# Kernel optimization log

Hardware: AMD Instinct MI355X
Metric: run time of the kernel (lower is better)

## Reference

```python
import jax, jax.numpy as jnp
import numpy as np

H = 64  # hidden_size


def _lstm_layer(xs, Wih, Whh, bih, bhh):
    # xs: (S, B, in_dim). PyTorch gate order: i, f, g, o.
    S, B, _ = xs.shape
    b = bih + bhh  # (4H,)
    # Precompute input projections for all timesteps (one big GEMM)
    x_proj = jnp.einsum('sbi,gi->sbg', xs, Wih) + b  # (S, B, 4H)

    def step(carry, xp_t):
        h, c = carry
        gates = xp_t + h @ Whh.T  # (B, 4H)
        i, f, g, o = jnp.split(gates, 4, axis=-1)
        i = jax.nn.sigmoid(i)
        f = jax.nn.sigmoid(f)
        g = jnp.tanh(g)
        o = jax.nn.sigmoid(o)
        c = f * c + i * g
        h = o * jnp.tanh(c)
        return (h, c), h

    h0 = jnp.zeros((B, H), dtype=xs.dtype)
    c0 = jnp.zeros((B, H), dtype=xs.dtype)
    _, ys = jax.lax.scan(step, (h0, c0), x_proj)
    return ys  # (S, B, H)


def setup_inputs() -> dict:
    key = jax.random.key(0)
    ks = jax.random.split(key, 16)
    scale = 1.0 / np.sqrt(H)  # PyTorch uniform(-1/sqrt(H), 1/sqrt(H)) scale

    def u(k, shape):
        return jax.random.uniform(k, shape, jnp.float32, -scale, scale)

    inp = {
        'x': jax.random.normal(ks[0], (512, 2048, 4), dtype=jnp.float32),
        # layer 0: input_size=4
        'Wih0': u(ks[1], (4 * H, 4)), 'Whh0': u(ks[2], (4 * H, H)),
        'bih0': u(ks[3], (4 * H,)), 'bhh0': u(ks[4], (4 * H,)),
        # layers 1,2: input_size=H
        'Wih1': u(ks[5], (4 * H, H)), 'Whh1': u(ks[6], (4 * H, H)),
        'bih1': u(ks[7], (4 * H,)), 'bhh1': u(ks[8], (4 * H,)),
        'Wih2': u(ks[9], (4 * H, H)), 'Whh2': u(ks[10], (4 * H, H)),
        'bih2': u(ks[11], (4 * H,)), 'bhh2': u(ks[12], (4 * H,)),
        # fc: Linear(64, 2)
        'fc_w': u(ks[13], (2, H)), 'fc_b': u(ks[14], (2,)),
    }
    return inp


def reference(x, Wih0, Whh0, bih0, bhh0, Wih1, Whh1, bih1, bhh1,
              Wih2, Whh2, bih2, bhh2, fc_w, fc_b):
    xs = jnp.transpose(x, (1, 0, 2))  # (S, B, 4) -- x.permute(1,0,2)
    h = _lstm_layer(xs, Wih0, Whh0, bih0, bhh0)
    h = _lstm_layer(h, Wih1, Whh1, bih1, bhh1)
    h = _lstm_layer(h, Wih2, Whh2, bih2, bhh2)
    last = h[-1]  # (B, H) -- out[-1]
    return last @ fc_w.T + fc_b  # (B, 2)
```

## Files before the change

### kernel.cpp

```cpp
#include <hip/hip_runtime.h>

#define SS 2048
#define BATCH 512
#define NB 2
#define NT 512

typedef float f2 __attribute__((ext_vector_type(2)));

__device__ __forceinline__ float fast_rcp(float a) { return __builtin_amdgcn_rcpf(a); }
__device__ __forceinline__ float fast_exp2(float a) { return __builtin_amdgcn_exp2f(a); }

__device__ __forceinline__ f2 pk_fma(f2 a, f2 b, f2 c) {
  return __builtin_elementwise_fma(a, b, c);
}
__device__ __forceinline__ f2 pk_mul(f2 a, f2 b) { return a * b; }

template <int CTRL>
__device__ __forceinline__ float dpp_add(float v) {
  const int sh = __builtin_amdgcn_update_dpp(0, __float_as_int(v), CTRL, 0xf, 0xf, true);
  return v + __int_as_float(sh);
}
template <int CTRL>
__device__ __forceinline__ float dpp_mov(float v) {
  return __int_as_float(__builtin_amdgcn_update_dpp(0, __float_as_int(v), CTRL, 0xf, 0xf, true));
}

__device__ __forceinline__ void lds_barrier() {
  asm volatile("s_waitcnt lgkmcnt(0)\n\ts_barrier" ::: "memory");
}

__device__ __forceinline__ void ld8(const float* p, f2 (&hv)[4]) {
  const float4 A = *(const float4*)p;
  const float4 B = *(const float4*)(p + 4);
  hv[0] = f2{A.x, A.y}; hv[1] = f2{A.z, A.w};
  hv[2] = f2{B.x, B.y}; hv[3] = f2{B.z, B.w};
}

__device__ __forceinline__ void mv8p_first(const f2 (&w)[4][4], const f2 (&hv)[4],
                                           f2 (&acc)[4]) {
#pragma unroll
  for (int g = 0; g < 4; ++g) {
    acc[g] = pk_mul(w[g][0], hv[0]);
#pragma unroll
    for (int k = 1; k < 4; ++k) acc[g] = pk_fma(w[g][k], hv[k], acc[g]);
  }
}
__device__ __forceinline__ void mv8p(const f2 (&w)[4][4], const f2 (&hv)[4],
                                     f2 (&acc)[4]) {
#pragma unroll
  for (int g = 0; g < 4; ++g) {
#pragma unroll
    for (int k = 0; k < 4; ++k) acc[g] = pk_fma(w[g][k], hv[k], acc[g]);
  }
}

__device__ __forceinline__ float redsel2(const f2 (&A)[4], const f2 (&B)[4],
                                         bool kb0, bool kb1, bool bsel) {
  float a[4], b[4];
#pragma unroll
  for (int g = 0; g < 4; ++g) { a[g] = A[g].x + A[g].y; b[g] = B[g].x + B[g].y; }
#pragma unroll
  for (int g = 0; g < 4; ++g) {
    a[g] = dpp_add<0xB1>(a[g]);
    a[g] = dpp_add<0x4E>(a[g]);
    b[g] = dpp_add<0xB1>(b[g]);
    b[g] = dpp_add<0x4E>(b[g]);
  }
  const float t0 = kb1 ? (kb0 ? a[3] : a[2]) : (kb0 ? a[1] : a[0]);
  const float t1 = kb1 ? (kb0 ? b[3] : b[2]) : (kb0 ? b[1] : b[0]);
  const float send = bsel ? t0 : t1;
  const float recv = dpp_mov<0x141>(send);
  const float own  = bsel ? t1 : t0;
  return own + recv;
}

__device__ __forceinline__ float gate_finish2(float pre, float kact, float aact,
                                              float bact, float& c, bool bsel) {
  const float e = fast_exp2(kact * pre);
  const float r = fast_rcp(1.0f + e);
  const float a = fmaf(aact, r, bact);
  const float u0 = dpp_mov<0x00>(a);
  const float u1 = dpp_mov<0x55>(a);
  const float u2 = dpp_mov<0xAA>(a);
  const float u3 = dpp_mov<0xFF>(a);
  const float prod = bsel ? (u3 * u1) : (u0 * u2);
  const float vf   = bsel ? u2 : u1;
  const float vo   = bsel ? u0 : u3;
  c = fmaf(vf, c, prod);
  const float te = fast_exp2(2.8853900817779268f * c);
  const float tr = fast_rcp(1.0f + te);
  const float t = vo * tr;
  return fmaf(-2.0f, t, vo);
}

template <int CUR, int NXT>
__device__ __forceinline__ void lstm_step(
    float (&hb)[2][3][NB][64],
    const f2 (&whh0)[4][4], const f2 (&wih1)[4][4],
    const f2 (&whh1)[4][4], const f2 (&wih2)[4][4],
    const f2 (&whh2)[4][4],
    const float (&wi0l)[4],
    float b0l, float b1l, float b2l,
    float kact, float aact, float bact,
    float& c0, float& c1, float& c2,
    const float (&xin)[NB][4], int j, int k0, int bi,
    bool kb0, bool kb1, bool bsel, bool wq,
    bool act0, bool act1, bool act2) {
  f2 p0[NB][4], p1[NB][4], p2[NB][4];
#pragma unroll
  for (int b = 0; b < NB; ++b) {
    f2 hv0[4], hv1[4], hv2[4];
    ld8(&hb[CUR][0][b][k0], hv0);
    ld8(&hb[CUR][1][b][k0], hv1);
    ld8(&hb[CUR][2][b][k0], hv2);
    mv8p_first(whh0, hv0, p0[b]);
    mv8p_first(wih1, hv0, p1[b]);
    mv8p      (whh1, hv1, p1[b]);
    mv8p_first(wih2, hv1, p2[b]);
    mv8p      (whh2, hv2, p2[b]);
  }
  {
    const float s = redsel2(p0[0], p0[1], kb0, kb1, bsel);
    float d = b0l;
#pragma unroll
    for (int f = 0; f < 4; ++f)
      d = fmaf(wi0l[f], bsel ? xin[1][f] : xin[0][f], d);
    float cc = c0;
    const float h = gate_finish2(s + d, kact, aact, bact, cc, bsel);
    if (act0) { c0 = cc; if (wq) hb[NXT][0][bi][j] = h; }
  }
  {
    const float s = redsel2(p1[0], p1[1], kb0, kb1, bsel);
    float cc = c1;
    const float h = gate_finish2(s + b1l, kact, aact, bact, cc, bsel);
    if (act1) { c1 = cc; if (wq) hb[NXT][1][bi][j] = h; }
  }
  {
    const float s = redsel2(p2[0], p2[1], kb0, kb1, bsel);
    float cc = c2;
    const float h = gate_finish2(s + b2l, kact, aact, bact, cc, bsel);
    if (act2) { c2 = cc; if (wq) hb[NXT][2][bi][j] = h; }
  }
  lds_barrier();
}

__global__ void __launch_bounds__(NT, 2)
lstm3_kernel(const float* __restrict__ x,
             const float* __restrict__ Wih0, const float* __restrict__ Whh0,
             const float* __restrict__ bih0, const float* __restrict__ bhh0,
             const float* __restrict__ Wih1, const float* __restrict__ Whh1,
             const float* __restrict__ bih1, const float* __restrict__ bhh1,
             const float* __restrict__ Wih2, const float* __restrict__ Whh2,
             const float* __restrict__ bih2, const float* __restrict__ bhh2,
             const float* __restrict__ fcw, const float* __restrict__ fcb,
             float* __restrict__ out) {
  __shared__ float hb[2][3][NB][64];
  const int tid = threadIdx.x;
  const int j = tid >> 3;
  const int ko = tid & 7;
  const int k0 = ko << 3;
  const int bbase = blockIdx.x * NB;
  const int gl = (ko & 4) ? (3 - (ko & 3)) : (ko & 3);
  const bool kb0 = (gl & 1) != 0;
  const bool kb1 = (gl & 2) != 0;
  const int  bi   = (ko >> 2) & 1;
  const bool bsel = bi != 0;
  const bool wq   = (ko & 3) == 0;

  f2 whh0[4][4], wih1[4][4], whh1[4][4], wih2[4][4], whh2[4][4];
#pragma unroll
  for (int g = 0; g < 4; ++g) {
    const int r = (g << 6) + j;
    const int ro = (r << 6) + k0;
#define LDW(dst, srcp)                                            \
    {                                                             \
      const float4 A = *(const float4*)&(srcp)[ro];               \
      const float4 B = *(const float4*)&(srcp)[ro + 4];           \
      dst[g][0] = f2{A.x, A.y}; dst[g][1] = f2{A.z, A.w};         \
      dst[g][2] = f2{B.x, B.y}; dst[g][3] = f2{B.z, B.w};         \
    }
    LDW(whh0, Whh0)
    LDW(wih1, Wih1)
    LDW(whh1, Whh1)
    LDW(wih2, Wih2)
    LDW(whh2, Whh2)
#undef LDW
  }

  const int rl = (gl << 6) + j;
  const float b0l = bih0[rl] + bhh0[rl];
  const float b1l = bih1[rl] + bhh1[rl];
  const float b2l = bih2[rl] + bhh2[rl];
  float wi0l[4];
  {
    const float4 w0 = *(const float4*)&Wih0[rl * 4];
    wi0l[0] = w0.x; wi0l[1] = w0.y; wi0l[2] = w0.z; wi0l[3] = w0.w;
  }
  const bool isg = (gl == 2);
  const float kact = isg ? 2.8853900817779268f : -1.4426950408889634f;
  const float aact = isg ? -2.0f : 1.0f;
  const float bact = isg ? 1.0f : 0.0f;

  float c0 = 0.f, c1 = 0.f, c2 = 0.f;

  {
    float* p = &hb[0][0][0][0];
    for (int i = tid; i < 2 * 3 * NB * 64; i += NT) p[i] = 0.f;
  }

  float xc[NB][4], xn[NB][4];
#pragma unroll
  for (int b = 0; b < NB; ++b) {
    const float4 v = *(const float4*)&x[(size_t)(bbase + b) * SS * 4];
    xc[b][0] = v.x; xc[b][1] = v.y; xc[b][2] = v.z; xc[b][3] = v.w;
  }
  __syncthreads();

#pragma unroll 1
  for (int t = 0; t < SS + 2; t += 2) {
    {
      const int i1 = (t + 1 < SS) ? (t + 1) : (SS - 1);
#pragma unroll
      for (int b = 0; b < NB; ++b) {
        const float4 v = *(const float4*)&x[((size_t)(bbase + b) * SS + i1) * 4];
        xn[b][0] = v.x; xn[b][1] = v.y; xn[b][2] = v.z; xn[b][3] = v.w;
      }
    }
    lstm_step<0, 1>(hb, whh0, wih1, whh1, wih2, whh2, wi0l, b0l, b1l, b2l,
                    kact, aact, bact, c0, c1, c2, xc, j, k0, bi,
                    kb0, kb1, bsel, wq,
                    t < SS, (t >= 1) && (t <= SS),
                    t >= 2);
    {
      const int i2 = (t + 2 < SS) ? (t + 2) : (SS - 1);
#pragma unroll
      for (int b = 0; b < NB; ++b) {
        const float4 v = *(const float4*)&x[((size_t)(bbase + b) * SS + i2) * 4];
        xc[b][0] = v.x; xc[b][1] = v.y; xc[b][2] = v.z; xc[b][3] = v.w;
      }
    }
    lstm_step<1, 0>(hb, whh0, wih1, whh1, wih2, whh2, wi0l, b0l, b1l, b2l,
                    kact, aact, bact, c0, c1, c2, xn, j, k0, bi,
                    kb0, kb1, bsel, wq,
                    t + 1 < SS, t + 1 <= SS,
                    t + 1 >= 2);
  }
  __syncthreads();

  if (tid < NB * 2) {
    const int b = tid >> 1, o = tid & 1;
    float s = fcb[o];
#pragma unroll
    for (int jj = 0; jj < 64; ++jj)
      s = fmaf(fcw[o * 64 + jj], hb[0][2][b][jj], s);
    out[(bbase + b) * 2 + o] = s;
  }
}

extern "C" void kernel_launch(void* const* d_in, const int* in_sizes, int n_in,
                              void* d_out, int out_size, void* d_ws, size_t ws_size,
                              hipStream_t stream) {
  const float* x    = (const float*)d_in[0];
  const float* Wih0 = (const float*)d_in[1];
  const float* Whh0 = (const float*)d_in[2];
  const float* bih0 = (const float*)d_in[3];
  const float* bhh0 = (const float*)d_in[4];
  const float* Wih1 = (const float*)d_in[5];
  const float* Whh1 = (const float*)d_in[6];
  const float* bih1 = (const float*)d_in[7];
  const float* bhh1 = (const float*)d_in[8];
  const float* Wih2 = (const float*)d_in[9];
  const float* Whh2 = (const float*)d_in[10];
  const float* bih2 = (const float*)d_in[11];
  const float* bhh2 = (const float*)d_in[12];
  const float* fcw  = (const float*)d_in[13];
  const float* fcb  = (const float*)d_in[14];
  float* out = (float*)d_out;

  lstm3_kernel<<<dim3(BATCH / NB), dim3(NT), 0, stream>>>(
      x, Wih0, Whh0, bih0, bhh0, Wih1, Whh1, bih1, bhh1,
      Wih2, Whh2, bih2, bhh2, fcw, fcb, out);
}
```

Measured before the change: 3.093 ms.

## Peel pipeline prologue/epilogue, pad LDS rows, and trim per-lane x loads

Moves the layer-activity predicates into template parameters and peels the first two and last two wavefront steps, so the steady-state loop carries no per-step activity checks. Pads the hidden-state LDS rows from 64 to 72 floats to reduce bank conflicts on the vectorized reads. Each lane now loads only its own batch row of x instead of both rows, and the DPP cross-lane move is fused into the add. These cut select and branch overhead and redundant loads on the serial recurrence path, at the cost of more code and a slightly larger shared buffer.

Result: faster. 2.864 ms (-7.4%).

```diff
diff --git a/kernel.cpp b/kernel.cpp
--- a/kernel.cpp
+++ b/kernel.cpp
@@ -4,6 +4,7 @@
 #define BATCH 512
 #define NB 2
 #define NT 512
+#define HS 72
 
 typedef float f2 __attribute__((ext_vector_type(2)));
 
@@ -20,9 +21,13 @@
   const int sh = __builtin_amdgcn_update_dpp(0, __float_as_int(v), CTRL, 0xf, 0xf, true);
   return v + __int_as_float(sh);
 }
+__device__ __forceinline__ float mirror_add(float s, float o) {
+  const int sh = __builtin_amdgcn_update_dpp(0, __float_as_int(s), 0x141, 0xf, 0xf, true);
+  return o + __int_as_float(sh);
+}
 template <int CTRL>
 __device__ __forceinline__ float dpp_mov(float v) {
-  return __int_as_float(__builtin_amdgcn_update_dpp(0, __float_as_int(v), CTRL, 0xf, 0xf, true));
+  return __int_as_float(__builtin_amdgcn_mov_dpp(__float_as_int(v), CTRL, 0xf, 0xf, true));
 }
 
 __device__ __forceinline__ void lds_barrier() {
@@ -69,9 +74,8 @@
   const float t0 = kb1 ? (kb0 ? a[3] : a[2]) : (kb0 ? a[1] : a[0]);
   const float t1 = kb1 ? (kb0 ? b[3] : b[2]) : (kb0 ? b[1] : b[0]);
   const float send = bsel ? t0 : t1;
-  const float recv = dpp_mov<0x141>(send);
   const float own  = bsel ? t1 : t0;
-  return own + recv;
+  return mirror_add(send, own);
 }
 
 __device__ __forceinline__ float gate_finish2(float pre, float kact, float aact,
@@ -93,9 +97,9 @@
   return fmaf(-2.0f, t, vo);
 }
 
-template <int CUR, int NXT>
+template <int CUR, int NXT, bool A0, bool A1, bool A2>
 __device__ __forceinline__ void lstm_step(
-    float (&hb)[2][3][NB][64],
+    float (&hb)[2][3][NB][HS],
     const f2 (&whh0)[4][4], const f2 (&wih1)[4][4],
     const f2 (&whh1)[4][4], const f2 (&wih2)[4][4],
     const f2 (&whh2)[4][4],
@@ -103,9 +107,9 @@
     float b0l, float b1l, float b2l,
     float kact, float aact, float bact,
     float& c0, float& c1, float& c2,
-    const float (&xin)[NB][4], int j, int k0, int bi,
-    bool kb0, bool kb1, bool bsel, bool wq,
-    bool act0, bool act1, bool act2) {
+    const float (&xin)[4],
+    int j, int k0, int bi,
+    bool kb0, bool kb1, bool bsel, bool wq) {
   f2 p0[NB][4], p1[NB][4], p2[NB][4];
 #pragma unroll
   for (int b = 0; b < NB; ++b) {
@@ -119,27 +123,29 @@
     mv8p_first(wih2, hv1, p2[b]);
     mv8p      (whh2, hv2, p2[b]);
   }
-  {
+  if (A0) {
     const float s = redsel2(p0[0], p0[1], kb0, kb1, bsel);
     float d = b0l;
 #pragma unroll
-    for (int f = 0; f < 4; ++f)
-      d = fmaf(wi0l[f], bsel ? xin[1][f] : xin[0][f], d);
+    for (int f = 0; f < 4; ++f) d = fmaf(wi0l[f], xin[f], d);
     float cc = c0;
     const float h = gate_finish2(s + d, kact, aact, bact, cc, bsel);
-    if (act0) { c0 = cc; if (wq) hb[NXT][0][bi][j] = h; }
-  }
-  {
+    c0 = cc;
+    if (wq) hb[NXT][0][bi][j] = h;
+  }
+  if (A1) {
     const float s = redsel2(p1[0], p1[1], kb0, kb1, bsel);
     float cc = c1;
     const float h = gate_finish2(s + b1l, kact, aact, bact, cc, bsel);
-    if (act1) { c1 = cc; if (wq) hb[NXT][1][bi][j] = h; }
-  }
-  {
+    c1 = cc;
+    if (wq) hb[NXT][1][bi][j] = h;
+  }
+  if (A2) {
     const float s = redsel2(p2[0], p2[1], kb0, kb1, bsel);
     float cc = c2;
     const float h = gate_finish2(s + b2l, kact, aact, bact, cc, bsel);
-    if (act2) { c2 = cc; if (wq) hb[NXT][2][bi][j] = h; }
+    c2 = cc;
+    if (wq) hb[NXT][2][bi][j] = h;
   }
   lds_barrier();
 }
@@ -154,7 +160,7 @@
              const float* __restrict__ bih2, const float* __restrict__ bhh2,
              const float* __restrict__ fcw, const float* __restrict__ fcb,
              float* __restrict__ out) {
-  __shared__ float hb[2][3][NB][64];
+  __shared__ __align__(16) float hb[2][3][NB][HS];
   const int tid = threadIdx.x;
   const int j = tid >> 3;
   const int ko = tid & 7;
@@ -205,46 +211,42 @@
 
   {
     float* p = &hb[0][0][0][0];
-    for (int i = tid; i < 2 * 3 * NB * 64; i += NT) p[i] = 0.f;
-  }
-
-  float xc[NB][4], xn[NB][4];
-#pragma unroll
-  for (int b = 0; b < NB; ++b) {
-    const float4 v = *(const float4*)&x[(size_t)(bbase + b) * SS * 4];
-    xc[b][0] = v.x; xc[b][1] = v.y; xc[b][2] = v.z; xc[b][3] = v.w;
+    for (int i = tid; i < 2 * 3 * NB * HS; i += NT) p[i] = 0.f;
+  }
+
+  const float* xlane = &x[(size_t)(bbase + bi) * SS * 4];
+  float xc[4], xn[4];
+  {
+    const float4 v = *(const float4*)xlane;
+    xc[0] = v.x; xc[1] = v.y; xc[2] = v.z; xc[3] = v.w;
   }
   __syncthreads();
 
+#define LOADX(dst, idx)                                           \
+  {                                                               \
+    const float4 v = *(const float4*)&xlane[(idx) * 4];           \
+    dst[0] = v.x; dst[1] = v.y; dst[2] = v.z; dst[3] = v.w;       \
+  }
+#define STEP(CUR, NXT, A0, A1, A2, xv)                                       \
+  lstm_step<CUR, NXT, A0, A1, A2>(hb, whh0, wih1, whh1, wih2, whh2, wi0l,    \
+                                  b0l, b1l, b2l, kact, aact, bact,           \
+                                  c0, c1, c2, xv, j, k0, bi, kb0, kb1,       \
+                                  bsel, wq)
+
+  LOADX(xn, 1)
+  STEP(0, 1, true, false, false, xc);
+  LOADX(xc, 2)
+  STEP(1, 0, true, true, false, xn);
 #pragma unroll 1
-  for (int t = 0; t < SS + 2; t += 2) {
-    {
-      const int i1 = (t + 1 < SS) ? (t + 1) : (SS - 1);
-#pragma unroll
-      for (int b = 0; b < NB; ++b) {
-        const float4 v = *(const float4*)&x[((size_t)(bbase + b) * SS + i1) * 4];
-        xn[b][0] = v.x; xn[b][1] = v.y; xn[b][2] = v.z; xn[b][3] = v.w;
-      }
-    }
-    lstm_step<0, 1>(hb, whh0, wih1, whh1, wih2, whh2, wi0l, b0l, b1l, b2l,
-                    kact, aact, bact, c0, c1, c2, xc, j, k0, bi,
-                    kb0, kb1, bsel, wq,
-                    t < SS, (t >= 1) && (t <= SS),
-                    t >= 2);
-    {
-      const int i2 = (t + 2 < SS) ? (t + 2) : (SS - 1);
-#pragma unroll
-      for (int b = 0; b < NB; ++b) {
-        const float4 v = *(const float4*)&x[((size_t)(bbase + b) * SS + i2) * 4];
-        xc[b][0] = v.x; xc[b][1] = v.y; xc[b][2] = v.z; xc[b][3] = v.w;
-      }
-    }
-    lstm_step<1, 0>(hb, whh0, wih1, whh1, wih2, whh2, wi0l, b0l, b1l, b2l,
-                    kact, aact, bact, c0, c1, c2, xn, j, k0, bi,
-                    kb0, kb1, bsel, wq,
-                    t + 1 < SS, t + 1 <= SS,
-                    t + 1 >= 2);
-  }
+  for (int t = 2; t < SS; t += 2) {
+    LOADX(xn, t + 1)
+    STEP(0, 1, true, true, true, xc);
+    const int tp = (t + 2 < SS) ? (t + 2) : (SS - 1);
+    LOADX(xc, tp)
+    STEP(1, 0, true, true, true, xn);
+  }
+  STEP(0, 1, false, true, true, xc);
+  STEP(1, 0, false, false, true, xn);
   __syncthreads();
 
   if (tid < NB * 2) {
@@ -255,6 +257,8 @@
       s = fmaf(fcw[o * 64 + jj], hb[0][2][b][jj], s);
     out[(bbase + b) * 2 + o] = s;
   }
+#undef LOADX
+#undef STEP
 }
 
 extern "C" void kernel_launch(void* const* d_in, const int* in_sizes, int n_in,
```
